# Kernel optimization log

Hardware: AMD Instinct MI355X
Metric: run time of the kernel (lower is better)

Reference implementation:

```python
import jax, jax.numpy as jnp
import numpy as np

N = 50000
E = 800000
IN_DIM = 512
HID = 256
OUT_DIM = 1


def gcn_conv(x, edge_index, W, b):
    # PyG GCNConv: add self-loops, symmetric normalization D^-1/2 A D^-1/2,
    # messages flow source (row) -> target (col), then linear transform + bias.
    n = x.shape[0]
    loop = jnp.arange(n, dtype=edge_index.dtype)
    src = jnp.concatenate([edge_index[0], loop])
    dst = jnp.concatenate([edge_index[1], loop])
    deg = jax.ops.segment_sum(jnp.ones_like(dst, dtype=x.dtype), dst, num_segments=n)
    dinv = jnp.where(deg > 0, jax.lax.rsqrt(deg), 0.0)
    norm = dinv[src] * dinv[dst]                      # [E+N]
    h = x @ W                                         # [N, out]
    msg = h[src] * norm[:, None]                      # [E+N, out] gather+scale
    out = jax.ops.segment_sum(msg, dst, num_segments=n)  # scatter-add
    return out + b


def setup_inputs() -> dict:
    key = jax.random.key(0)
    ks = jax.random.split(key, 8)
    x = jax.random.normal(ks[0], (N, IN_DIM), dtype=jnp.float32)
    edge_index = jax.random.randint(ks[1], (2, E), 0, N, dtype=jnp.int64)
    s1 = 1.0 / np.sqrt(IN_DIM)
    s2 = 1.0 / np.sqrt(HID)
    W1 = jax.random.uniform(ks[2], (IN_DIM, HID), jnp.float32, -s1, s1)
    b1 = jnp.zeros((HID,), jnp.float32)
    W2 = jax.random.uniform(ks[3], (HID, HID), jnp.float32, -s2, s2)
    b2 = jnp.zeros((HID,), jnp.float32)
    Wfc = jax.random.uniform(ks[4], (HID, OUT_DIM), jnp.float32, -s2, s2)
    bfc = jax.random.uniform(ks[5], (OUT_DIM,), jnp.float32, -s2, s2)
    return {"x": x, "edge_index": edge_index, "W1": W1, "b1": b1,
            "W2": W2, "b2": b2, "Wfc": Wfc, "bfc": bfc}


def reference(x, edge_index, W1, b1, W2, b2, Wfc, bfc):
    h = jax.nn.relu(gcn_conv(x, edge_index, W1, b1))
    h = jax.nn.relu(gcn_conv(h, edge_index, W2, b2))
    g = jnp.mean(h, axis=0)                           # [HID] graph readout
    return jax.nn.sigmoid(g @ Wfc + bfc)              # [OUT_DIM]
```

## Files before the change

### kernel.cpp

```cpp
#include <hip/hip_runtime.h>
#include <stdint.h>

#define AS1 __attribute__((address_space(1)))
#define AS3 __attribute__((address_space(3)))

typedef __bf16 bf16x8 __attribute__((ext_vector_type(8)));
typedef float  f32x4  __attribute__((ext_vector_type(4)));
typedef unsigned short u16x8 __attribute__((ext_vector_type(8)));

static constexpr int NODES  = 50000;
static constexpr int EDGES  = 800000;
static constexpr int INDIM  = 512;
static constexpr int HIDDIM = 256;
static constexpr int NB_SCAN = (NODES + 255) / 256;
static constexpr int AGG_BLOCKS = NODES / 4;
static constexpr int RED_BLOCKS = 64;
static constexpr int GEMM_MB256 = (NODES + 255) / 256;

static constexpr size_t OFF_PART = 0;
static constexpr size_t OFF_HN   = 51200000;
static constexpr size_t OFF_H1P  = 76800000;
static constexpr size_t OFF_W1T  = 102400000;
static constexpr size_t OFF_W2T  = 102662144;
static constexpr size_t OFF_DEG  = 102793216;
static constexpr size_t OFF_FILL = 102993216;
static constexpr size_t OFF_ROWP = 103193216;
static constexpr size_t OFF_CSR  = 103393280;
static constexpr size_t OFF_BSUM = 106593280;
static constexpr size_t OFF_BOFF = 106594304;
static constexpr size_t OFF_P2   = 106595840;
static constexpr size_t OFF_DINV = 106661376;

__device__ __forceinline__ unsigned short f2bf(float f) {
  unsigned u = __builtin_bit_cast(unsigned, f);
  unsigned r = (u + 0x7FFFu + ((u >> 16) & 1u)) >> 16;
  return (unsigned short)r;
}
__device__ __forceinline__ float bf2f(unsigned short u) {
  return __builtin_bit_cast(float, ((unsigned)u) << 16);
}
__device__ __forceinline__ unsigned char f2fp8(float f) {
  int p = __builtin_amdgcn_cvt_pk_fp8_f32(f, f, 0, false);
  return (unsigned char)(p & 0xff);
}
__device__ __forceinline__ void acc_fp8(float4& a, unsigned u) {
  a.x += __builtin_amdgcn_cvt_f32_fp8(u, 0);
  a.y += __builtin_amdgcn_cvt_f32_fp8(u, 1);
  a.z += __builtin_amdgcn_cvt_f32_fp8(u, 2);
  a.w += __builtin_amdgcn_cvt_f32_fp8(u, 3);
}
__device__ __forceinline__ void gload_lds16(const unsigned short* g, unsigned short* l) {
  __builtin_amdgcn_global_load_lds((const AS1 void*)g, (AS3 void*)l, 16, 0, 0);
}

#define WAITVM(N)  asm volatile("s_waitcnt vmcnt(" #N ")" ::: "memory")
#define WAITLGKM   asm volatile("s_waitcnt lgkmcnt(0)" ::: "memory")
#define HWBARRIER  { asm volatile("" ::: "memory"); __builtin_amdgcn_s_barrier(); \
                     asm volatile("" ::: "memory"); }

__global__ __launch_bounds__(256) void transw_zero_kernel(const float* __restrict__ W1,
                                                          const float* __restrict__ W2,
                                                          unsigned short* __restrict__ W1T,
                                                          unsigned short* __restrict__ W2T,
                                                          int4* __restrict__ zreg) {
  int b = blockIdx.x, tid = threadIdx.x;
  if (b < 512) {
    int t = b * 256 + tid; int n = t >> 9, k = t & 511;
    W1T[t] = f2bf(W1[k * HIDDIM + n]);
  } else if (b < 768) {
    int u = (b - 512) * 256 + tid; int n = u >> 8, k = u & 255;
    W2T[u] = f2bf(W2[k * HIDDIM + n]);
  } else {
    int i = (b - 768) * 256 + tid;
    if (i < 25000) zreg[i] = int4{0, 0, 0, 0};
  }
}

__global__ __launch_bounds__(256) void hist_kernel(const int* __restrict__ ei,
                                                   int* __restrict__ deg) {
  __shared__ int sflag;
  if (threadIdx.x < 64) {
    unsigned long long b = __ballot(ei[2 * threadIdx.x + 1] == 0);
    if (threadIdx.x == 0) sflag = (b == 0xFFFFFFFFFFFFFFFFull) ? 1 : 0;
  }
  __syncthreads();
  int f = sflag;
  int e = blockIdx.x * 256 + threadIdx.x;
  int d = f ? ei[2 * (EDGES + e)] : ei[EDGES + e];
  atomicAdd(&deg[d], 1);
}

__global__ __launch_bounds__(256) void scan1_kernel(const int* __restrict__ deg,
                                                    int* __restrict__ rowptr,
                                                    int* __restrict__ bsum,
                                                    float* __restrict__ dinv) {
  __shared__ int s[256];
  int t = threadIdx.x, i = blockIdx.x * 256 + t;
  int v = (i < NODES) ? deg[i] : 0;
  if (i < NODES) dinv[i] = rsqrtf((float)(v + 1));
  s[t] = v; __syncthreads();
  for (int off = 1; off < 256; off <<= 1) {
    int x = (t >= off) ? s[t - off] : 0;
    __syncthreads(); s[t] += x; __syncthreads();
  }
  if (i < NODES) rowptr[i] = s[t] - v;
  if (t == 255) bsum[blockIdx.x] = s[255];
}
__global__ __launch_bounds__(256) void scan2_kernel(const int* __restrict__ bsum,
                                                    int* __restrict__ boff,
                                                    int* __restrict__ rowptrN) {
  __shared__ int s[256];
  int t = threadIdx.x;
  int v = (t < NB_SCAN) ? bsum[t] : 0;
  s[t] = v; __syncthreads();
  for (int off = 1; off < 256; off <<= 1) {
    int x = (t >= off) ? s[t - off] : 0;
    __syncthreads(); s[t] += x; __syncthreads();
  }
  if (t < NB_SCAN) boff[t] = s[t] - v;
  if (t == 255) *rowptrN = s[255];
}
__global__ __launch_bounds__(256) void scan3_kernel(int* __restrict__ rowptr,
                                                    const int* __restrict__ boff) {
  int i = blockIdx.x * 256 + threadIdx.x;
  if (i < NODES) rowptr[i] += boff[blockIdx.x];
}

__global__ __launch_bounds__(256) void fill_kernel(const int* __restrict__ ei,
                                                   const int* __restrict__ rowptr,
                                                   int* __restrict__ fill,
                                                   int* __restrict__ csr) {
  __shared__ int sflag;
  if (threadIdx.x < 64) {
    unsigned long long b = __ballot(ei[2 * threadIdx.x + 1] == 0);
    if (threadIdx.x == 0) sflag = (b == 0xFFFFFFFFFFFFFFFFull) ? 1 : 0;
  }
  __syncthreads();
  int f = sflag;
  int e = blockIdx.x * 256 + threadIdx.x;
  int s, d;
  if (f) { s = ei[2 * e]; d = ei[2 * (EDGES + e)]; }
  else   { s = ei[e];     d = ei[EDGES + e]; }
  int p = atomicAdd(&fill[d], 1);
  csr[rowptr[d] + p] = s;
}

template<int K, bool AFP32>
__global__ __launch_bounds__(512, 2) void gemm_m256_kernel(const void* __restrict__ Av,
                                                           const unsigned short* __restrict__ BT,
                                                           const float* __restrict__ dinv,
                                                           unsigned char* __restrict__ Cn8) {
  constexpr int NSTEP = K / 32;
  __shared__ unsigned short As[2][256 * 32];
  __shared__ unsigned short Bs[2][256 * 32];
  const int tid = threadIdx.x, wave = tid >> 6, lane = tid & 63;
  const int fr = lane & 15, q = lane >> 4;
  const int wr = wave >> 2, wc = wave & 3;
  const int m0 = blockIdx.x * 256;

  const int lrow4 = lane >> 2;
  const int sgq   = (lane & 3) ^ (lrow4 & 3);
  const unsigned short* a16 = (const unsigned short*)Av;
  const float*          a32 = (const float*)Av;

  f32x4 acc[8][4] = {};
  float4 fa[4];

#define STAGE_B(buf, kb)                                                      \
  {                                                                           \
    _Pragma("unroll")                                                         \
    for (int c = 0; c < 2; ++c) {                                             \
      int rbase = wave * 32 + c * 16;                                         \
      int gr = rbase + lrow4;                                                 \
      gload_lds16(BT + (size_t)gr * K + (kb) + sgq * 8, &Bs[buf][rbase * 32]);\
    }                                                                         \
  }
#define STAGE_A16(buf, kb)                                                    \
  {                                                                           \
    _Pragma("unroll")                                                         \
    for (int c = 0; c < 2; ++c) {                                             \
      int rbase = wave * 32 + c * 16;                                         \
      int gr = m0 + rbase + lrow4; if (gr > NODES - 1) gr = NODES - 1;        \
      gload_lds16(a16 + (size_t)gr * K + (kb) + sgq * 8, &As[buf][rbase * 32]);\
    }                                                                         \
  }
#define LOAD_A32(kb)                                                          \
  {                                                                           \
    _Pragma("unroll")                                                         \
    for (int j = 0; j < 4; ++j) {                                             \
      int F = tid + j * 512;                                                  \
      int r0 = m0 + (F >> 3); if (r0 > NODES - 1) r0 = NODES - 1;             \
      fa[j] = *(const float4*)(a32 + (size_t)r0 * K + (kb) + (F & 7) * 4);    \
    }                                                                         \
  }
#define WRITE_A32(buf)                                                        \
  {                                                                           \
    _Pragma("unroll")                                                         \
    for (int j = 0; j < 4; ++j) {                                             \
      int F = tid + j * 512;                                                  \
      int row = F >> 3, g4 = F & 7;                                           \
      ushort4 o{f2bf(fa[j].x), f2bf(fa[j].y), f2bf(fa[j].z), f2bf(fa[j].w)};  \
      int col = (((g4 >> 1) ^ (row & 3)) * 8) + (g4 & 1) * 4;                 \
      *(ushort4*)&As[buf][row * 32 + col] = o;                                \
    }                                                                         \
  }

  if constexpr (AFP32) { LOAD_A32(0); WRITE_A32(0); WAITLGKM; }
  else                 { STAGE_A16(0, 0); }
  STAGE_B(0, 0);

  for (int t = 0; t < NSTEP; ++t) {
    const int cur = t & 1, nxt = cur ^ 1;
    if (t + 1 < NSTEP) {
      const int kb1 = (t + 1) * 32;
      if constexpr (AFP32) { LOAD_A32(kb1); } else { STAGE_A16(nxt, kb1); }
      STAGE_B(nxt, kb1);
      if constexpr (AFP32) { WAITVM(6); } else { WAITVM(4); }
    } else {
      WAITVM(0);
    }
    HWBARRIER;

    bf16x8 af[8], bq[4];
#pragma unroll
    for (int m = 0; m < 8; ++m) {
      int row = wr * 128 + m * 16 + fr;
      af[m] = *(const bf16x8*)&As[cur][row * 32 + ((q ^ (row & 3)) * 8)];
    }
#pragma unroll
    for (int n = 0; n < 4; ++n) {
      int row = wc * 64 + n * 16 + fr;
      bq[n] = *(const bf16x8*)&Bs[cur][row * 32 + ((q ^ (row & 3)) * 8)];
    }
#pragma unroll
    for (int m = 0; m < 8; ++m)
#pragma unroll
      for (int n = 0; n < 4; ++n)
        acc[m][n] = __builtin_amdgcn_mfma_f32_16x16x32_bf16(af[m], bq[n], acc[m][n], 0, 0, 0);

    if (t + 1 < NSTEP) {
      if constexpr (AFP32) { WRITE_A32(nxt); WAITLGKM; }
    }
    HWBARRIER;
  }
#undef STAGE_B
#undef STAGE_A16
#undef LOAD_A32
#undef WRITE_A32

  const int rq = q * 4;
#pragma unroll
  for (int m = 0; m < 8; ++m) {
    int rbase = m0 + wr * 128 + m * 16 + rq;
#pragma unroll
    for (int r = 0; r < 4; ++r) {
      int grow = rbase + r;
      if (grow < NODES) {
        float dv = dinv[grow];
#pragma unroll
        for (int n = 0; n < 4; ++n) {
          int gcol = wc * 64 + n * 16 + fr;
          Cn8[(size_t)grow * 256 + gcol] = f2fp8(acc[m][n][r] * dv);
        }
      }
    }
  }
}

__device__ __forceinline__ float4 gather_node(const unsigned char* __restrict__ hn8,
                                              const int* __restrict__ rowptr,
                                              const int* __restrict__ csr,
                                              int node, int boff) {
  float4 A{0.f, 0.f, 0.f, 0.f}, B{0.f, 0.f, 0.f, 0.f};
  unsigned us = *(const unsigned*)(hn8 + (size_t)node * 256 + boff);
  acc_fp8(A, us);
  int e0 = rowptr[node], e1 = rowptr[node + 1];
  int e = e0;
  for (; e + 8 <= e1; e += 8) {
    unsigned u0 = *(const unsigned*)(hn8 + (size_t)csr[e + 0] * 256 + boff);
    unsigned u1 = *(const unsigned*)(hn8 + (size_t)csr[e + 1] * 256 + boff);
    unsigned u2 = *(const unsigned*)(hn8 + (size_t)csr[e + 2] * 256 + boff);
    unsigned u3 = *(const unsigned*)(hn8 + (size_t)csr[e + 3] * 256 + boff);
    unsigned u4 = *(const unsigned*)(hn8 + (size_t)csr[e + 4] * 256 + boff);
    unsigned u5 = *(const unsigned*)(hn8 + (size_t)csr[e + 5] * 256 + boff);
    unsigned u6 = *(const unsigned*)(hn8 + (size_t)csr[e + 6] * 256 + boff);
    unsigned u7 = *(const unsigned*)(hn8 + (size_t)csr[e + 7] * 256 + boff);
    acc_fp8(A, u0); acc_fp8(B, u1); acc_fp8(A, u2); acc_fp8(B, u3);
    acc_fp8(A, u4); acc_fp8(B, u5); acc_fp8(A, u6); acc_fp8(B, u7);
  }
  for (; e + 4 <= e1; e += 4) {
    unsigned u0 = *(const unsigned*)(hn8 + (size_t)csr[e + 0] * 256 + boff);
    unsigned u1 = *(const unsigned*)(hn8 + (size_t)csr[e + 1] * 256 + boff);
    unsigned u2 = *(const unsigned*)(hn8 + (size_t)csr[e + 2] * 256 + boff);
    unsigned u3 = *(const unsigned*)(hn8 + (size_t)csr[e + 3] * 256 + boff);
    acc_fp8(A, u0); acc_fp8(B, u1); acc_fp8(A, u2); acc_fp8(B, u3);
  }
  for (; e < e1; ++e) {
    unsigned u = *(const unsigned*)(hn8 + (size_t)csr[e] * 256 + boff);
    acc_fp8(A, u);
  }
  return float4{A.x + B.x, A.y + B.y, A.z + B.z, A.w + B.w};
}

__global__ __launch_bounds__(256) void agg1_kernel(const unsigned char* __restrict__ hn8,
                                                   const float* __restrict__ dinv,
                                                   const int* __restrict__ rowptr,
                                                   const int* __restrict__ csr,
                                                   const float* __restrict__ bias,
                                                   unsigned short* __restrict__ outp) {
  int wave = threadIdx.x >> 6, lane = threadIdx.x & 63;
  int node = blockIdx.x * 4 + wave;
  int c0 = lane * 4;
  float4 a = gather_node(hn8, rowptr, csr, node, c0);
  float di = dinv[node];
  float4 b = *(const float4*)(bias + c0);
  ushort4 o{f2bf(fmaxf(fmaf(di, a.x, b.x), 0.f)),
            f2bf(fmaxf(fmaf(di, a.y, b.y), 0.f)),
            f2bf(fmaxf(fmaf(di, a.z, b.z), 0.f)),
            f2bf(fmaxf(fmaf(di, a.w, b.w), 0.f))};
  *(ushort4*)(outp + (size_t)node * 256 + c0) = o;
}

__global__ __launch_bounds__(256) void agg2_kernel(const unsigned char* __restrict__ hn8,
                                                   const float* __restrict__ dinv,
                                                   const int* __restrict__ rowptr,
                                                   const int* __restrict__ csr,
                                                   const float* __restrict__ bias,
                                                   float* __restrict__ partials) {
  __shared__ float sm[1024];
  int wave = threadIdx.x >> 6, lane = threadIdx.x & 63;
  int node = blockIdx.x * 4 + wave;
  int c0 = lane * 4;
  float4 a = gather_node(hn8, rowptr, csr, node, c0);
  float di = dinv[node];
  float4 b = *(const float4*)(bias + c0);
  sm[wave * 256 + c0 + 0] = fmaxf(fmaf(di, a.x, b.x), 0.f);
  sm[wave * 256 + c0 + 1] = fmaxf(fmaf(di, a.y, b.y), 0.f);
  sm[wave * 256 + c0 + 2] = fmaxf(fmaf(di, a.z, b.z), 0.f);
  sm[wave * 256 + c0 + 3] = fmaxf(fmaf(di, a.w, b.w), 0.f);
  __syncthreads();
  int t = threadIdx.x;
  partials[(size_t)blockIdx.x * 256 + t] = sm[t] + sm[256 + t] + sm[512 + t] + sm[768 + t];
}

__global__ __launch_bounds__(256) void reduce2_kernel(const float* __restrict__ partials,
                                                      float* __restrict__ p2) {
  int t = threadIdx.x, b = blockIdx.x;
  float s = 0.f;
  for (int r = b; r < AGG_BLOCKS; r += RED_BLOCKS) s += partials[(size_t)r * 256 + t];
  p2[b * 256 + t] = s;
}
__global__ __launch_bounds__(256) void final_kernel(const float* __restrict__ p2,
                                                    const float* __restrict__ Wfc,
                                                    const float* __restrict__ bfc,
                                                    float* __restrict__ out) {
  __shared__ float red[256];
  int t = threadIdx.x;
  float s = 0.f;
  for (int b = 0; b < RED_BLOCKS; ++b) s += p2[b * 256 + t];
  float g = s * (1.0f / (float)NODES);
  red[t] = g * Wfc[t];
  __syncthreads();
  for (int off = 128; off > 0; off >>= 1) {
    if (t < off) red[t] += red[t + off];
    __syncthreads();
  }
  if (t == 0) {
    float z = red[0] + bfc[0];
    out[0] = 1.0f / (1.0f + expf(-z));
  }
}

extern "C" void kernel_launch(void* const* d_in, const int* in_sizes, int n_in,
                              void* d_out, int out_size, void* d_ws, size_t ws_size,
                              hipStream_t stream) {
  (void)in_sizes; (void)n_in; (void)out_size; (void)ws_size;
  const float* x   = (const float*)d_in[0];
  const int*   ei  = (const int*)d_in[1];
  const float* W1  = (const float*)d_in[2];
  const float* b1  = (const float*)d_in[3];
  const float* W2  = (const float*)d_in[4];
  const float* b2  = (const float*)d_in[5];
  const float* Wfc = (const float*)d_in[6];
  const float* bfc = (const float*)d_in[7];
  float* out = (float*)d_out;
  char* ws = (char*)d_ws;

  unsigned char*  hn8  = (unsigned char*)(ws + OFF_HN);
  unsigned short* h1p  = (unsigned short*)(ws + OFF_H1P);
  unsigned short* w1t  = (unsigned short*)(ws + OFF_W1T);
  unsigned short* w2t  = (unsigned short*)(ws + OFF_W2T);
  int*   deg    = (int*)(ws + OFF_DEG);
  int*   fill   = (int*)(ws + OFF_FILL);
  int*   rowptr = (int*)(ws + OFF_ROWP);
  int*   csr    = (int*)(ws + OFF_CSR);
  int*   bsum   = (int*)(ws + OFF_BSUM);
  int*   boff   = (int*)(ws + OFF_BOFF);
  float* part   = (float*)(ws + OFF_PART);
  float* p2     = (float*)(ws + OFF_P2);
  float* dinv   = (float*)(ws + OFF_DINV);

  transw_zero_kernel<<<866, 256, 0, stream>>>(W1, W2, w1t, w2t, (int4*)deg);
  hist_kernel<<<EDGES / 256, 256, 0, stream>>>(ei, deg);
  scan1_kernel<<<NB_SCAN, 256, 0, stream>>>(deg, rowptr, bsum, dinv);
  scan2_kernel<<<1, 256, 0, stream>>>(bsum, boff, rowptr + NODES);
  scan3_kernel<<<NB_SCAN, 256, 0, stream>>>(rowptr, boff);
  fill_kernel<<<EDGES / 256, 256, 0, stream>>>(ei, rowptr, fill, csr);

  gemm_m256_kernel<INDIM, true><<<GEMM_MB256, 512, 0, stream>>>(x, w1t, dinv, hn8);
  agg1_kernel<<<AGG_BLOCKS, 256, 0, stream>>>(hn8, dinv, rowptr, csr, b1, h1p);
  gemm_m256_kernel<HIDDIM, false><<<GEMM_MB256, 512, 0, stream>>>(h1p, w2t, dinv, hn8);
  agg2_kernel<<<AGG_BLOCKS, 256, 0, stream>>>(hn8, dinv, rowptr, csr, b2, part);
  reduce2_kernel<<<RED_BLOCKS, 256, 0, stream>>>(part, p2);
  final_kernel<<<1, 256, 0, stream>>>(p2, Wfc, bfc, out);
}
```

Baseline: 271.4 us.

## Store GEMM operands in fp8 and convert to bf16 in registers before MFMA

Adds a pre-pass that converts x from fp32 to fp8, and stores the transposed weights and the layer-1 activations as fp8 instead of bf16. The GEMM now stages fp8 tiles (64 K per step) directly into LDS with global_load_lds and widens them to bf16 in registers before the bf16 MFMAs. This cuts the bytes each GEMM reads, for A, B and the intermediate h1. In exchange it adds a separate full pass over x, extra conversion ALU work in the GEMM inner loop, and a large precision loss from quantising inputs and weights to fp8.

```diff
diff --git a/kernel.cpp b/kernel.cpp
--- a/kernel.cpp
+++ b/kernel.cpp
@@ -6,7 +6,6 @@
 
 typedef __bf16 bf16x8 __attribute__((ext_vector_type(8)));
 typedef float  f32x4  __attribute__((ext_vector_type(4)));
-typedef unsigned short u16x8 __attribute__((ext_vector_type(8)));
 
 static constexpr int NODES  = 50000;
 static constexpr int EDGES  = 800000;
@@ -31,14 +30,6 @@
 static constexpr size_t OFF_P2   = 106595840;
 static constexpr size_t OFF_DINV = 106661376;
 
-__device__ __forceinline__ unsigned short f2bf(float f) {
-  unsigned u = __builtin_bit_cast(unsigned, f);
-  unsigned r = (u + 0x7FFFu + ((u >> 16) & 1u)) >> 16;
-  return (unsigned short)r;
-}
-__device__ __forceinline__ float bf2f(unsigned short u) {
-  return __builtin_bit_cast(float, ((unsigned)u) << 16);
-}
 __device__ __forceinline__ unsigned char f2fp8(float f) {
   int p = __builtin_amdgcn_cvt_pk_fp8_f32(f, f, 0, false);
   return (unsigned char)(p & 0xff);
@@ -49,27 +40,52 @@
   a.z += __builtin_amdgcn_cvt_f32_fp8(u, 2);
   a.w += __builtin_amdgcn_cvt_f32_fp8(u, 3);
 }
-__device__ __forceinline__ void gload_lds16(const unsigned short* g, unsigned short* l) {
+__device__ __forceinline__ void gload_lds8(const unsigned char* g, unsigned char* l) {
   __builtin_amdgcn_global_load_lds((const AS1 void*)g, (AS3 void*)l, 16, 0, 0);
 }
+__device__ __forceinline__ bf16x8 fp8x8_to_bf16x8(unsigned long long v) {
+  unsigned lo = (unsigned)v, hi = (unsigned)(v >> 32);
+  float f0 = __builtin_amdgcn_cvt_f32_fp8(lo, 0), f1 = __builtin_amdgcn_cvt_f32_fp8(lo, 1);
+  float f2 = __builtin_amdgcn_cvt_f32_fp8(lo, 2), f3 = __builtin_amdgcn_cvt_f32_fp8(lo, 3);
+  float f4 = __builtin_amdgcn_cvt_f32_fp8(hi, 0), f5 = __builtin_amdgcn_cvt_f32_fp8(hi, 1);
+  float f6 = __builtin_amdgcn_cvt_f32_fp8(hi, 2), f7 = __builtin_amdgcn_cvt_f32_fp8(hi, 3);
+  unsigned r0, r1, r2, r3;
+  asm("v_cvt_pk_bf16_f32 %0, %1, %2" : "=v"(r0) : "v"(f0), "v"(f1));
+  asm("v_cvt_pk_bf16_f32 %0, %1, %2" : "=v"(r1) : "v"(f2), "v"(f3));
+  asm("v_cvt_pk_bf16_f32 %0, %1, %2" : "=v"(r2) : "v"(f4), "v"(f5));
+  asm("v_cvt_pk_bf16_f32 %0, %1, %2" : "=v"(r3) : "v"(f6), "v"(f7));
+  uint4 u{r0, r1, r2, r3};
+  return __builtin_bit_cast(bf16x8, u);
+}
 
 #define WAITVM(N)  asm volatile("s_waitcnt vmcnt(" #N ")" ::: "memory")
-#define WAITLGKM   asm volatile("s_waitcnt lgkmcnt(0)" ::: "memory")
 #define HWBARRIER  { asm volatile("" ::: "memory"); __builtin_amdgcn_s_barrier(); \
                      asm volatile("" ::: "memory"); }
 
-__global__ __launch_bounds__(256) void transw_zero_kernel(const float* __restrict__ W1,
-                                                          const float* __restrict__ W2,
-                                                          unsigned short* __restrict__ W1T,
-                                                          unsigned short* __restrict__ W2T,
-                                                          int4* __restrict__ zreg) {
+__global__ __launch_bounds__(256) void convx8_kernel(const float* __restrict__ x,
+                                                     unsigned char* __restrict__ x8) {
+  size_t i = (size_t)(blockIdx.x * 256 + threadIdx.x) * 8;
+  float4 v0 = *(const float4*)(x + i);
+  float4 v1 = *(const float4*)(x + i + 4);
+  int p0 = __builtin_amdgcn_cvt_pk_fp8_f32(v0.x, v0.y, 0, false);
+  p0     = __builtin_amdgcn_cvt_pk_fp8_f32(v0.z, v0.w, p0, true);
+  int p1 = __builtin_amdgcn_cvt_pk_fp8_f32(v1.x, v1.y, 0, false);
+  p1     = __builtin_amdgcn_cvt_pk_fp8_f32(v1.z, v1.w, p1, true);
+  *(uint2*)(x8 + i) = uint2{(unsigned)p0, (unsigned)p1};
+}
+
+__global__ __launch_bounds__(256) void transw8_zero_kernel(const float* __restrict__ W1,
+                                                           const float* __restrict__ W2,
+                                                           unsigned char* __restrict__ W1T8,
+                                                           unsigned char* __restrict__ W2T8,
+                                                           int4* __restrict__ zreg) {
   int b = blockIdx.x, tid = threadIdx.x;
   if (b < 512) {
     int t = b * 256 + tid; int n = t >> 9, k = t & 511;
-    W1T[t] = f2bf(W1[k * HIDDIM + n]);
+    W1T8[t] = f2fp8(W1[k * HIDDIM + n]);
   } else if (b < 768) {
     int u = (b - 512) * 256 + tid; int n = u >> 8, k = u & 255;
-    W2T[u] = f2bf(W2[k * HIDDIM + n]);
+    W2T8[u] = f2fp8(W2[k * HIDDIM + n]);
   } else {
     int i = (b - 768) * 256 + tid;
     if (i < 25000) zreg[i] = int4{0, 0, 0, 0};
@@ -145,108 +161,79 @@
   csr[rowptr[d] + p] = s;
 }
 
-template<int K, bool AFP32>
-__global__ __launch_bounds__(512, 2) void gemm_m256_kernel(const void* __restrict__ Av,
-                                                           const unsigned short* __restrict__ BT,
-                                                           const float* __restrict__ dinv,
-                                                           unsigned char* __restrict__ Cn8) {
-  constexpr int NSTEP = K / 32;
-  __shared__ unsigned short As[2][256 * 32];
-  __shared__ unsigned short Bs[2][256 * 32];
+template<int K>
+__global__ __launch_bounds__(512, 2) void gemm_fp8_kernel(const unsigned char* __restrict__ A8,
+                                                          const unsigned char* __restrict__ BT8,
+                                                          const float* __restrict__ dinv,
+                                                          unsigned char* __restrict__ Cn8) {
+  constexpr int NSTEP = K / 64;
+  __shared__ unsigned char As[2][256 * 64];
+  __shared__ unsigned char Bs[2][256 * 64];
   const int tid = threadIdx.x, wave = tid >> 6, lane = tid & 63;
   const int fr = lane & 15, q = lane >> 4;
   const int wr = wave >> 2, wc = wave & 3;
   const int m0 = blockIdx.x * 256;
 
-  const int lrow4 = lane >> 2;
-  const int sgq   = (lane & 3) ^ (lrow4 & 3);
-  const unsigned short* a16 = (const unsigned short*)Av;
-  const float*          a32 = (const float*)Av;
+  const int srl0 = lane >> 2, sch = lane & 3;
 
   f32x4 acc[8][4] = {};
-  float4 fa[4];
-
-#define STAGE_B(buf, kb)                                                      \
+
+#define STAGE_T(dstArr, buf, srcp, rowbase, kb, CLAMP)                        \
   {                                                                           \
     _Pragma("unroll")                                                         \
     for (int c = 0; c < 2; ++c) {                                             \
-      int rbase = wave * 32 + c * 16;                                         \
-      int gr = rbase + lrow4;                                                 \
-      gload_lds16(BT + (size_t)gr * K + (kb) + sgq * 8, &Bs[buf][rbase * 32]);\
+      int rl = (wave * 2 + c) * 16 + srl0;                                    \
+      int gr = (rowbase) + rl;                                                \
+      if (CLAMP) { if (gr > NODES - 1) gr = NODES - 1; }                      \
+      const unsigned char* sp = srcp + (size_t)gr * K + (kb) +                \
+                                ((sch ^ (rl & 3)) << 4);                      \
+      gload_lds8(sp, &dstArr[buf][(wave * 2 + c) * 1024]);                    \
     }                                                                         \
   }
-#define STAGE_A16(buf, kb)                                                    \
-  {                                                                           \
-    _Pragma("unroll")                                                         \
-    for (int c = 0; c < 2; ++c) {                                             \
-      int rbase = wave * 32 + c * 16;                                         \
-      int gr = m0 + rbase + lrow4; if (gr > NODES - 1) gr = NODES - 1;        \
-      gload_lds16(a16 + (size_t)gr * K + (kb) + sgq * 8, &As[buf][rbase * 32]);\
-    }                                                                         \
-  }
-#define LOAD_A32(kb)                                                          \
-  {                                                                           \
-    _Pragma("unroll")                                                         \
-    for (int j = 0; j < 4; ++j) {                                             \
-      int F = tid + j * 512;                                                  \
-      int r0 = m0 + (F >> 3); if (r0 > NODES - 1) r0 = NODES - 1;             \
-      fa[j] = *(const float4*)(a32 + (size_t)r0 * K + (kb) + (F & 7) * 4);    \
-    }                                                                         \
-  }
-#define WRITE_A32(buf)                                                        \
-  {                                                                           \
-    _Pragma("unroll")                                                         \
-    for (int j = 0; j < 4; ++j) {                                             \
-      int F = tid + j * 512;                                                  \
-      int row = F >> 3, g4 = F & 7;                                           \
-      ushort4 o{f2bf(fa[j].x), f2bf(fa[j].y), f2bf(fa[j].z), f2bf(fa[j].w)};  \
-      int col = (((g4 >> 1) ^ (row & 3)) * 8) + (g4 & 1) * 4;                 \
-      *(ushort4*)&As[buf][row * 32 + col] = o;                                \
-    }                                                                         \
-  }
-
-  if constexpr (AFP32) { LOAD_A32(0); WRITE_A32(0); WAITLGKM; }
-  else                 { STAGE_A16(0, 0); }
-  STAGE_B(0, 0);
+
+  STAGE_T(As, 0, A8, m0, 0, true);
+  STAGE_T(Bs, 0, BT8, 0, 0, false);
 
   for (int t = 0; t < NSTEP; ++t) {
     const int cur = t & 1, nxt = cur ^ 1;
     if (t + 1 < NSTEP) {
-      const int kb1 = (t + 1) * 32;
-      if constexpr (AFP32) { LOAD_A32(kb1); } else { STAGE_A16(nxt, kb1); }
-      STAGE_B(nxt, kb1);
-      if constexpr (AFP32) { WAITVM(6); } else { WAITVM(4); }
+      const int kb1 = (t + 1) * 64;
+      STAGE_T(As, nxt, A8, m0, kb1, true);
+      STAGE_T(Bs, nxt, BT8, 0, kb1, false);
+      WAITVM(4);
     } else {
       WAITVM(0);
     }
     HWBARRIER;
 
-    bf16x8 af[8], bq[4];
-#pragma unroll
-    for (int m = 0; m < 8; ++m) {
-      int row = wr * 128 + m * 16 + fr;
-      af[m] = *(const bf16x8*)&As[cur][row * 32 + ((q ^ (row & 3)) * 8)];
-    }
-#pragma unroll
-    for (int n = 0; n < 4; ++n) {
-      int row = wc * 64 + n * 16 + fr;
-      bq[n] = *(const bf16x8*)&Bs[cur][row * 32 + ((q ^ (row & 3)) * 8)];
-    }
-#pragma unroll
-    for (int m = 0; m < 8; ++m)
-#pragma unroll
-      for (int n = 0; n < 4; ++n)
-        acc[m][n] = __builtin_amdgcn_mfma_f32_16x16x32_bf16(af[m], bq[n], acc[m][n], 0, 0, 0);
-
-    if (t + 1 < NSTEP) {
-      if constexpr (AFP32) { WRITE_A32(nxt); WAITLGKM; }
+#pragma unroll
+    for (int s = 0; s < 2; ++s) {
+      bf16x8 af[8], bq[4];
+#pragma unroll
+      for (int m = 0; m < 8; ++m) {
+        int row = wr * 128 + m * 16 + fr;
+        int cch = s * 2 + (q >> 1);
+        unsigned long long v = *(const unsigned long long*)
+            &As[cur][row * 64 + ((cch ^ (row & 3)) << 4) + (q & 1) * 8];
+        af[m] = fp8x8_to_bf16x8(v);
+      }
+#pragma unroll
+      for (int n = 0; n < 4; ++n) {
+        int row = wc * 64 + n * 16 + fr;
+        int cch = s * 2 + (q >> 1);
+        unsigned long long v = *(const unsigned long long*)
+            &Bs[cur][row * 64 + ((cch ^ (row & 3)) << 4) + (q & 1) * 8];
+        bq[n] = fp8x8_to_bf16x8(v);
+      }
+#pragma unroll
+      for (int m = 0; m < 8; ++m)
+#pragma unroll
+        for (int n = 0; n < 4; ++n)
+          acc[m][n] = __builtin_amdgcn_mfma_f32_16x16x32_bf16(af[m], bq[n], acc[m][n], 0, 0, 0);
     }
     HWBARRIER;
   }
-#undef STAGE_B
-#undef STAGE_A16
-#undef LOAD_A32
-#undef WRITE_A32
+#undef STAGE_T
 
   const int rq = q * 4;
 #pragma unroll
@@ -307,18 +294,20 @@
                                                    const int* __restrict__ rowptr,
                                                    const int* __restrict__ csr,
                                                    const float* __restrict__ bias,
-                                                   unsigned short* __restrict__ outp) {
+                                                   unsigned char* __restrict__ h1p8) {
   int wave = threadIdx.x >> 6, lane = threadIdx.x & 63;
   int node = blockIdx.x * 4 + wave;
   int c0 = lane * 4;
   float4 a = gather_node(hn8, rowptr, csr, node, c0);
   float di = dinv[node];
   float4 b = *(const float4*)(bias + c0);
-  ushort4 o{f2bf(fmaxf(fmaf(di, a.x, b.x), 0.f)),
-            f2bf(fmaxf(fmaf(di, a.y, b.y), 0.f)),
-            f2bf(fmaxf(fmaf(di, a.z, b.z), 0.f)),
-            f2bf(fmaxf(fmaf(di, a.w, b.w), 0.f))};
-  *(ushort4*)(outp + (size_t)node * 256 + c0) = o;
+  float r0 = fmaxf(fmaf(di, a.x, b.x), 0.f);
+  float r1 = fmaxf(fmaf(di, a.y, b.y), 0.f);
+  float r2 = fmaxf(fmaf(di, a.z, b.z), 0.f);
+  float r3 = fmaxf(fmaf(di, a.w, b.w), 0.f);
+  int p = __builtin_amdgcn_cvt_pk_fp8_f32(r0, r1, 0, false);
+  p     = __builtin_amdgcn_cvt_pk_fp8_f32(r2, r3, p, true);
+  *(unsigned*)(h1p8 + (size_t)node * 256 + c0) = (unsigned)p;
 }
 
 __global__ __launch_bounds__(256) void agg2_kernel(const unsigned char* __restrict__ hn8,
@@ -387,9 +376,10 @@
   char* ws = (char*)d_ws;
 
   unsigned char*  hn8  = (unsigned char*)(ws + OFF_HN);
-  unsigned short* h1p  = (unsigned short*)(ws + OFF_H1P);
-  unsigned short* w1t  = (unsigned short*)(ws + OFF_W1T);
-  unsigned short* w2t  = (unsigned short*)(ws + OFF_W2T);
+  unsigned char*  x8   = (unsigned char*)(ws + OFF_H1P);
+  unsigned char*  h1p8 = (unsigned char*)(ws + OFF_H1P);
+  unsigned char*  w1t8 = (unsigned char*)(ws + OFF_W1T);
+  unsigned char*  w2t8 = (unsigned char*)(ws + OFF_W2T);
   int*   deg    = (int*)(ws + OFF_DEG);
   int*   fill   = (int*)(ws + OFF_FILL);
   int*   rowptr = (int*)(ws + OFF_ROWP);
@@ -400,16 +390,17 @@
   float* p2     = (float*)(ws + OFF_P2);
   float* dinv   = (float*)(ws + OFF_DINV);
 
-  transw_zero_kernel<<<866, 256, 0, stream>>>(W1, W2, w1t, w2t, (int4*)deg);
+  transw8_zero_kernel<<<866, 256, 0, stream>>>(W1, W2, w1t8, w2t8, (int4*)deg);
   hist_kernel<<<EDGES / 256, 256, 0, stream>>>(ei, deg);
   scan1_kernel<<<NB_SCAN, 256, 0, stream>>>(deg, rowptr, bsum, dinv);
   scan2_kernel<<<1, 256, 0, stream>>>(bsum, boff, rowptr + NODES);
   scan3_kernel<<<NB_SCAN, 256, 0, stream>>>(rowptr, boff);
   fill_kernel<<<EDGES / 256, 256, 0, stream>>>(ei, rowptr, fill, csr);
-
-  gemm_m256_kernel<INDIM, true><<<GEMM_MB256, 512, 0, stream>>>(x, w1t, dinv, hn8);
-  agg1_kernel<<<AGG_BLOCKS, 256, 0, stream>>>(hn8, dinv, rowptr, csr, b1, h1p);
-  gemm_m256_kernel<HIDDIM, false><<<GEMM_MB256, 512, 0, stream>>>(h1p, w2t, dinv, hn8);
+  convx8_kernel<<<NODES * INDIM / (256 * 8), 256, 0, stream>>>(x, x8);
+
+  gemm_fp8_kernel<INDIM><<<GEMM_MB256, 512, 0, stream>>>(x8, w1t8, dinv, hn8);
+  agg1_kernel<<<AGG_BLOCKS, 256, 0, stream>>>(hn8, dinv, rowptr, csr, b1, h1p8);
+  gemm_fp8_kernel<HIDDIM><<<GEMM_MB256, 512, 0, stream>>>(h1p8, w2t8, dinv, hn8);
   agg2_kernel<<<AGG_BLOCKS, 256, 0, stream>>>(hn8, dinv, rowptr, csr, b2, part);
   reduce2_kernel<<<RED_BLOCKS, 256, 0, stream>>>(part, p2);
   final_kernel<<<1, 256, 0, stream>>>(p2, Wfc, bfc, out);
```

Result: slower. 291.3 us (+7.4%).

## Split GEMMs into 128-row tiles with triple-buffered LDS pipelines

Applied to the files above, without the earlier changes.

Replaces the shared templated 256-row GEMM with two specialized kernels that use 128-row M tiles and a three-stage LDS ring buffer, prefetching two K-steps ahead. The layer-1 kernel double-registers the fp32 A loads so conversion to bf16 overlaps the next loads. Smaller tiles double the block count, giving more CUs work on 50000 rows. The cost is more reloads of B per row and lower MFMA reuse per block.

```diff
diff --git a/kernel.cpp b/kernel.cpp
--- a/kernel.cpp
+++ b/kernel.cpp
@@ -6,7 +6,6 @@
 
 typedef __bf16 bf16x8 __attribute__((ext_vector_type(8)));
 typedef float  f32x4  __attribute__((ext_vector_type(4)));
-typedef unsigned short u16x8 __attribute__((ext_vector_type(8)));
 
 static constexpr int NODES  = 50000;
 static constexpr int EDGES  = 800000;
@@ -15,7 +14,7 @@
 static constexpr int NB_SCAN = (NODES + 255) / 256;
 static constexpr int AGG_BLOCKS = NODES / 4;
 static constexpr int RED_BLOCKS = 64;
-static constexpr int GEMM_MB256 = (NODES + 255) / 256;
+static constexpr int GEMM_MB128 = (NODES + 127) / 128;
 
 static constexpr size_t OFF_PART = 0;
 static constexpr size_t OFF_HN   = 51200000;
@@ -35,9 +34,6 @@
   unsigned u = __builtin_bit_cast(unsigned, f);
   unsigned r = (u + 0x7FFFu + ((u >> 16) & 1u)) >> 16;
   return (unsigned short)r;
-}
-__device__ __forceinline__ float bf2f(unsigned short u) {
-  return __builtin_bit_cast(float, ((unsigned)u) << 16);
 }
 __device__ __forceinline__ unsigned char f2fp8(float f) {
   int p = __builtin_amdgcn_cvt_pk_fp8_f32(f, f, 0, false);
@@ -145,126 +141,166 @@
   csr[rowptr[d] + p] = s;
 }
 
-template<int K, bool AFP32>
-__global__ __launch_bounds__(512, 2) void gemm_m256_kernel(const void* __restrict__ Av,
-                                                           const unsigned short* __restrict__ BT,
-                                                           const float* __restrict__ dinv,
-                                                           unsigned char* __restrict__ Cn8) {
-  constexpr int NSTEP = K / 32;
-  __shared__ unsigned short As[2][256 * 32];
-  __shared__ unsigned short Bs[2][256 * 32];
+
+#define G_COMPUTE(cur)                                                        \
+  {                                                                           \
+    bf16x8 af[4], bq[4];                                                      \
+    _Pragma("unroll")                                                         \
+    for (int m = 0; m < 4; ++m) {                                             \
+      int row = wr * 64 + m * 16 + fr;                                        \
+      af[m] = *(const bf16x8*)&As[(cur) * 4096 + row * 32 + ((q ^ (row & 3)) * 8)]; \
+    }                                                                         \
+    _Pragma("unroll")                                                         \
+    for (int n = 0; n < 4; ++n) {                                             \
+      int row = wc * 64 + n * 16 + fr;                                        \
+      bq[n] = *(const bf16x8*)&Bs[(cur) * 8192 + row * 32 + ((q ^ (row & 3)) * 8)]; \
+    }                                                                         \
+    _Pragma("unroll")                                                         \
+    for (int m = 0; m < 4; ++m)                                               \
+      _Pragma("unroll")                                                       \
+      for (int n = 0; n < 4; ++n)                                             \
+        acc[m][n] = __builtin_amdgcn_mfma_f32_16x16x32_bf16(af[m], bq[n], acc[m][n], 0, 0, 0); \
+  }
+
+#define G_EPILOGUE                                                            \
+  {                                                                           \
+    const int rq = q * 4;                                                     \
+    _Pragma("unroll")                                                         \
+    for (int m = 0; m < 4; ++m) {                                             \
+      int rbase = m0 + wr * 64 + m * 16 + rq;                                 \
+      _Pragma("unroll")                                                       \
+      for (int r = 0; r < 4; ++r) {                                           \
+        int grow = rbase + r;                                                 \
+        if (grow < NODES) {                                                   \
+          float dv = dinv[grow];                                              \
+          _Pragma("unroll")                                                   \
+          for (int n = 0; n < 4; ++n) {                                       \
+            int gcol = wc * 64 + n * 16 + fr;                                 \
+            Cn8[(size_t)grow * 256 + gcol] = f2fp8(acc[m][n][r] * dv);        \
+          }                                                                   \
+        }                                                                     \
+      }                                                                       \
+    }                                                                         \
+  }
+
+#define G_STAGEB(buf, kb)                                                     \
+  {                                                                           \
+    _Pragma("unroll")                                                         \
+    for (int j = 0; j < 2; ++j) {                                             \
+      int F = tid + j * 512;                                                  \
+      int row = F >> 2, g = F & 3;                                            \
+      gload_lds16(BT + (size_t)row * K + (kb) + ((g ^ (row & 3)) * 8),        \
+                  Bs + (buf) * 8192 + F * 8);                                 \
+    }                                                                         \
+  }
+
+__global__ __launch_bounds__(512, 2) void gemm1_deep(const float* __restrict__ A,
+                                                     const unsigned short* __restrict__ BT,
+                                                     const float* __restrict__ dinv,
+                                                     unsigned char* __restrict__ Cn8) {
+  constexpr int K = INDIM, NSTEP = K / 32;
+  __shared__ unsigned short As[3 * 128 * 32];
+  __shared__ unsigned short Bs[3 * 256 * 32];
   const int tid = threadIdx.x, wave = tid >> 6, lane = tid & 63;
   const int fr = lane & 15, q = lane >> 4;
   const int wr = wave >> 2, wc = wave & 3;
-  const int m0 = blockIdx.x * 256;
-
-  const int lrow4 = lane >> 2;
-  const int sgq   = (lane & 3) ^ (lrow4 & 3);
-  const unsigned short* a16 = (const unsigned short*)Av;
-  const float*          a32 = (const float*)Av;
-
-  f32x4 acc[8][4] = {};
-  float4 fa[4];
-
-#define STAGE_B(buf, kb)                                                      \
-  {                                                                           \
-    _Pragma("unroll")                                                         \
-    for (int c = 0; c < 2; ++c) {                                             \
-      int rbase = wave * 32 + c * 16;                                         \
-      int gr = rbase + lrow4;                                                 \
-      gload_lds16(BT + (size_t)gr * K + (kb) + sgq * 8, &Bs[buf][rbase * 32]);\
-    }                                                                         \
-  }
-#define STAGE_A16(buf, kb)                                                    \
-  {                                                                           \
-    _Pragma("unroll")                                                         \
-    for (int c = 0; c < 2; ++c) {                                             \
-      int rbase = wave * 32 + c * 16;                                         \
-      int gr = m0 + rbase + lrow4; if (gr > NODES - 1) gr = NODES - 1;        \
-      gload_lds16(a16 + (size_t)gr * K + (kb) + sgq * 8, &As[buf][rbase * 32]);\
-    }                                                                         \
-  }
-#define LOAD_A32(kb)                                                          \
-  {                                                                           \
-    _Pragma("unroll")                                                         \
-    for (int j = 0; j < 4; ++j) {                                             \
+  const int m0 = blockIdx.x * 128;
+
+  f32x4 acc[4][4] = {};
+  float4 fa0[2], fa1[2];
+
+#define G1_LOADA(fa, kb)                                                      \
+  {                                                                           \
+    _Pragma("unroll")                                                         \
+    for (int j = 0; j < 2; ++j) {                                             \
       int F = tid + j * 512;                                                  \
-      int r0 = m0 + (F >> 3); if (r0 > NODES - 1) r0 = NODES - 1;             \
-      fa[j] = *(const float4*)(a32 + (size_t)r0 * K + (kb) + (F & 7) * 4);    \
-    }                                                                         \
-  }
-#define WRITE_A32(buf)                                                        \
-  {                                                                           \
-    _Pragma("unroll")                                                         \
-    for (int j = 0; j < 4; ++j) {                                             \
+      int row = F >> 3;                                                       \
+      int gr = m0 + row; if (gr > NODES - 1) gr = NODES - 1;                  \
+      fa[j] = *(const float4*)(A + (size_t)gr * K + (kb) + (F & 7) * 4);      \
+    }                                                                         \
+  }
+#define G1_WRITEA(buf, fa)                                                    \
+  {                                                                           \
+    _Pragma("unroll")                                                         \
+    for (int j = 0; j < 2; ++j) {                                             \
       int F = tid + j * 512;                                                  \
-      int row = F >> 3, g4 = F & 7;                                           \
+      int row = F >> 3, g8 = F & 7;                                           \
       ushort4 o{f2bf(fa[j].x), f2bf(fa[j].y), f2bf(fa[j].z), f2bf(fa[j].w)};  \
-      int col = (((g4 >> 1) ^ (row & 3)) * 8) + (g4 & 1) * 4;                 \
-      *(ushort4*)&As[buf][row * 32 + col] = o;                                \
-    }                                                                         \
-  }
-
-  if constexpr (AFP32) { LOAD_A32(0); WRITE_A32(0); WAITLGKM; }
-  else                 { STAGE_A16(0, 0); }
-  STAGE_B(0, 0);
+      int col = (((g8 >> 1) ^ (row & 3)) * 8) + (g8 & 1) * 4;                 \
+      *(ushort4*)&As[(buf) * 4096 + row * 32 + col] = o;                      \
+    }                                                                         \
+  }
+#define G1_BODY(t, faH, faL)                                                  \
+  {                                                                           \
+    if ((t) + 2 < NSTEP) {                                                    \
+      G1_LOADA(faL, ((t) + 2) * 32);                                          \
+      G_STAGEB(((t) + 2) % 3, ((t) + 2) * 32);                                \
+      WAITVM(8);                                                              \
+    } else if ((t) + 1 < NSTEP) { WAITVM(4); } else { WAITVM(0); }            \
+    HWBARRIER;                                                                \
+    G_COMPUTE((t) % 3);                                                       \
+    if ((t) + 1 < NSTEP) { G1_WRITEA(((t) + 1) % 3, faH); WAITLGKM; }         \
+    HWBARRIER;                                                                \
+  }
+
+  G1_LOADA(fa0, 0);
+  G_STAGEB(0, 0);
+  G1_WRITEA(0, fa0);
+  G1_LOADA(fa1, 32);
+  G_STAGEB(1, 32);
+  WAITLGKM;
+
+  for (int tt = 0; tt < NSTEP; tt += 2) {
+    G1_BODY(tt,     fa1, fa0);
+    G1_BODY(tt + 1, fa0, fa1);
+  }
+#undef G1_LOADA
+#undef G1_WRITEA
+#undef G1_BODY
+
+  G_EPILOGUE;
+}
+
+__global__ __launch_bounds__(512, 2) void gemm2_deep(const unsigned short* __restrict__ A16,
+                                                     const unsigned short* __restrict__ BT,
+                                                     const float* __restrict__ dinv,
+                                                     unsigned char* __restrict__ Cn8) {
+  constexpr int K = HIDDIM, NSTEP = K / 32;
+  __shared__ unsigned short As[3 * 128 * 32];
+  __shared__ unsigned short Bs[3 * 256 * 32];
+  const int tid = threadIdx.x, wave = tid >> 6, lane = tid & 63;
+  const int fr = lane & 15, q = lane >> 4;
+  const int wr = wave >> 2, wc = wave & 3;
+  const int m0 = blockIdx.x * 128;
+
+  f32x4 acc[4][4] = {};
+
+#define G2_STAGEA(buf, kb)                                                    \
+  {                                                                           \
+    int row = tid >> 2, g = tid & 3;                                          \
+    int gr = m0 + row; if (gr > NODES - 1) gr = NODES - 1;                    \
+    gload_lds16(A16 + (size_t)gr * K + (kb) + ((g ^ (row & 3)) * 8),          \
+                As + (buf) * 4096 + tid * 8);                                 \
+  }
+
+  G2_STAGEA(0, 0);
+  G_STAGEB(0, 0);
+  G2_STAGEA(1, 32);
+  G_STAGEB(1, 32);
 
   for (int t = 0; t < NSTEP; ++t) {
-    const int cur = t & 1, nxt = cur ^ 1;
-    if (t + 1 < NSTEP) {
-      const int kb1 = (t + 1) * 32;
-      if constexpr (AFP32) { LOAD_A32(kb1); } else { STAGE_A16(nxt, kb1); }
-      STAGE_B(nxt, kb1);
-      if constexpr (AFP32) { WAITVM(6); } else { WAITVM(4); }
-    } else {
-      WAITVM(0);
-    }
+    if (t + 2 < NSTEP) {
+      G2_STAGEA((t + 2) % 3, (t + 2) * 32);
+      G_STAGEB((t + 2) % 3, (t + 2) * 32);
+      WAITVM(6);
+    } else if (t + 1 < NSTEP) { WAITVM(3); } else { WAITVM(0); }
     HWBARRIER;
-
-    bf16x8 af[8], bq[4];
-#pragma unroll
-    for (int m = 0; m < 8; ++m) {
-      int row = wr * 128 + m * 16 + fr;
-      af[m] = *(const bf16x8*)&As[cur][row * 32 + ((q ^ (row & 3)) * 8)];
-    }
-#pragma unroll
-    for (int n = 0; n < 4; ++n) {
-      int row = wc * 64 + n * 16 + fr;
-      bq[n] = *(const bf16x8*)&Bs[cur][row * 32 + ((q ^ (row & 3)) * 8)];
-    }
-#pragma unroll
-    for (int m = 0; m < 8; ++m)
-#pragma unroll
-      for (int n = 0; n < 4; ++n)
-        acc[m][n] = __builtin_amdgcn_mfma_f32_16x16x32_bf16(af[m], bq[n], acc[m][n], 0, 0, 0);
-
-    if (t + 1 < NSTEP) {
-      if constexpr (AFP32) { WRITE_A32(nxt); WAITLGKM; }
-    }
+    G_COMPUTE(t % 3);
     HWBARRIER;
   }
-#undef STAGE_B
-#undef STAGE_A16
-#undef LOAD_A32
-#undef WRITE_A32
-
-  const int rq = q * 4;
-#pragma unroll
-  for (int m = 0; m < 8; ++m) {
-    int rbase = m0 + wr * 128 + m * 16 + rq;
-#pragma unroll
-    for (int r = 0; r < 4; ++r) {
-      int grow = rbase + r;
-      if (grow < NODES) {
-        float dv = dinv[grow];
-#pragma unroll
-        for (int n = 0; n < 4; ++n) {
-          int gcol = wc * 64 + n * 16 + fr;
-          Cn8[(size_t)grow * 256 + gcol] = f2fp8(acc[m][n][r] * dv);
-        }
-      }
-    }
-  }
+#undef G2_STAGEA
+
+  G_EPILOGUE;
 }
 
 __device__ __forceinline__ float4 gather_node(const unsigned char* __restrict__ hn8,
@@ -407,9 +443,9 @@
   scan3_kernel<<<NB_SCAN, 256, 0, stream>>>(rowptr, boff);
   fill_kernel<<<EDGES / 256, 256, 0, stream>>>(ei, rowptr, fill, csr);
 
-  gemm_m256_kernel<INDIM, true><<<GEMM_MB256, 512, 0, stream>>>(x, w1t, dinv, hn8);
+  gemm1_deep<<<GEMM_MB128, 512, 0, stream>>>(x, w1t, dinv, hn8);
   agg1_kernel<<<AGG_BLOCKS, 256, 0, stream>>>(hn8, dinv, rowptr, csr, b1, h1p);
-  gemm_m256_kernel<HIDDIM, false><<<GEMM_MB256, 512, 0, stream>>>(h1p, w2t, dinv, hn8);
+  gemm2_deep<<<GEMM_MB128, 512, 0, stream>>>(h1p, w2t, dinv, hn8);
   agg2_kernel<<<AGG_BLOCKS, 256, 0, stream>>>(hn8, dinv, rowptr, csr, b2, part);
   reduce2_kernel<<<RED_BLOCKS, 256, 0, stream>>>(part, p2);
   final_kernel<<<1, 256, 0, stream>>>(p2, Wfc, bfc, out);
```

New measurement: 275.9 us. No clear change (+1.7%).
